# Kernel tuning notes

Hardware: AMD Instinct MI355X
Metric: run time of the kernel (lower is better)

## Reference

```python
import jax, jax.numpy as jnp
import numpy as np


def setup_inputs() -> dict:
    key = jax.random.key(0)
    k1, k2, k3, k4 = jax.random.split(key, 4)
    B, S, D = 2, 2048, 1024
    return {
        "X": jax.random.normal(k1, (B, S, D), dtype=jnp.float32),
        "W_q": jax.random.normal(k2, (D, D), dtype=jnp.float32),
        "W_k": jax.random.normal(k3, (D, D), dtype=jnp.float32),
        "W_v": jax.random.normal(k4, (D, D), dtype=jnp.float32),
        "n_heads": 16,
    }


def reference(X, W_q, W_k, W_v, n_heads):
    B, S, D = X.shape
    H = n_heads
    dh = D // H
    # QKV projections, split heads: [B,S,D] -> [H,B,S,dh]
    def split_heads(Y):
        return Y.reshape(B, S, H, dh).transpose(2, 0, 1, 3)
    Q = split_heads(X @ W_q)
    K = split_heads(X @ W_k)
    V = split_heads(X @ W_v)
    scale = 1.0 / jnp.sqrt(jnp.asarray(dh, dtype=X.dtype))
    # [H,B,S,S] attention scores (naive, matches the original)
    scores = jax.nn.softmax(jnp.einsum("hbqd,hbkd->hbqk", Q, K) * scale, axis=-1)
    out = jnp.einsum("hbqk,hbkd->hbqd", scores, V)  # [H,B,S,dh]
    # torch.concat(out, 0) over leading H dim -> [H*B, S, dh]
    return out.reshape(H * B, S, dh)
```

## Files before the change

kernel.cpp:

```cpp
#include <hip/hip_runtime.h>

typedef unsigned short u16;
typedef unsigned int u32;
typedef __bf16 bf16x8 __attribute__((ext_vector_type(8)));
typedef float f32x4 __attribute__((ext_vector_type(4)));
typedef float f32x16 __attribute__((ext_vector_type(16)));

extern "C" __device__ float __ocml_native_exp2_f32(float);

#define WT_HI_E  ((size_t)0)
#define WT_LO_E  ((size_t)3 << 20)
#define X_HI_E   ((size_t)6 << 20)
#define X_LO_E   ((size_t)10 << 20)
#define Q_HI_E   ((size_t)14 << 20)
#define Q_LO_E   ((size_t)18 << 20)
#define K_HI_E   ((size_t)22 << 20)
#define K_LO_E   ((size_t)26 << 20)
#define V_HI_E   ((size_t)30 << 20)
#define ML_BYTE  (17u << 20)

__device__ __forceinline__ u16 bf16_rne(float x) {
  u32 u = __float_as_uint(x);
  u32 r = (u + 0x7fffu + ((u >> 16) & 1u)) >> 16;
  return (u16)r;
}
__device__ __forceinline__ float bf16_f(u16 h) {
  return __uint_as_float(((u32)h) << 16);
}
__device__ __forceinline__ u16 f2bf(float x) {
  __bf16 b = (__bf16)x;
  return __builtin_bit_cast(u16, b);
}

__device__ __forceinline__ void gload16(const u16* g, u16* l) {
  __builtin_amdgcn_global_load_lds(
      (const __attribute__((address_space(1))) void*)g,
      (__attribute__((address_space(3))) void*)l, 16, 0, 0);
}

__global__ __launch_bounds__(256) void k_split(const float* __restrict__ X,
                                               const float* __restrict__ w0,
                                               const float* __restrict__ w1,
                                               const float* __restrict__ w2,
                                               u16* __restrict__ ws) {
  int bid = blockIdx.x;
  if (bid < 2048) {
    u16* xh = ws + X_HI_E;
    u16* xl = ws + X_LO_E;
    size_t i = ((size_t)bid * 256 + threadIdx.x) * 8;
    float4 a = *(const float4*)(X + i);
    float4 b = *(const float4*)(X + i + 4);
    float v[8] = {a.x, a.y, a.z, a.w, b.x, b.y, b.z, b.w};
    u32 Hh[4], Ll[4];
#pragma unroll
    for (int j = 0; j < 4; j++) {
      u16 h0 = f2bf(v[2 * j]);
      u16 h1 = f2bf(v[2 * j + 1]);
      u16 l0 = f2bf(v[2 * j] - bf16_f(h0));
      u16 l1 = f2bf(v[2 * j + 1] - bf16_f(h1));
      Hh[j] = (u32)h0 | ((u32)h1 << 16);
      Ll[j] = (u32)l0 | ((u32)l1 << 16);
    }
    *(uint4*)(xh + i) = make_uint4(Hh[0], Hh[1], Hh[2], Hh[3]);
    *(uint4*)(xl + i) = make_uint4(Ll[0], Ll[1], Ll[2], Ll[3]);
  } else {
    int wb = bid - 2048;
    int z = wb >> 8;
    int rem = wb & 255;
    int by = (rem >> 4) * 64, bx = (rem & 15) * 64;
    const float* W = (z == 0) ? w0 : ((z == 1) ? w1 : w2);
    u16* th = ws + WT_HI_E + (size_t)z * (1u << 20);
    u16* tl = ws + WT_LO_E + (size_t)z * (1u << 20);
    __shared__ float tile[64][65];
    int tx = threadIdx.x & 15, ty = threadIdx.x >> 4;
#pragma unroll
    for (int i = 0; i < 4; i++) {
      int r = ty + i * 16;
      float4 v = *(const float4*)(W + (size_t)(by + r) * 1024 + bx + tx * 4);
      tile[r][tx * 4 + 0] = v.x;
      tile[r][tx * 4 + 1] = v.y;
      tile[r][tx * 4 + 2] = v.z;
      tile[r][tx * 4 + 3] = v.w;
    }
    __syncthreads();
#pragma unroll
    for (int p = 0; p < 2; p++) {
      int t = threadIdx.x + 256 * p;
      int kc = t & 7, nl = t >> 3;
      u32 Hh[4], Ll[4];
#pragma unroll
      for (int u = 0; u < 4; u++) {
        float v0 = tile[kc * 8 + 2 * u][nl];
        float v1 = tile[kc * 8 + 2 * u + 1][nl];
        u16 h0 = f2bf(v0);
        u16 h1 = f2bf(v1);
        u16 l0 = f2bf(v0 - bf16_f(h0));
        u16 l1 = f2bf(v1 - bf16_f(h1));
        Hh[u] = (u32)h0 | ((u32)h1 << 16);
        Ll[u] = (u32)l0 | ((u32)l1 << 16);
      }
      size_t o = (size_t)(bx + nl) * 1024 + by + kc * 8;
      *(uint4*)(th + o) = make_uint4(Hh[0], Hh[1], Hh[2], Hh[3]);
      *(uint4*)(tl + o) = make_uint4(Ll[0], Ll[1], Ll[2], Ll[3]);
    }
  }
}

__global__ __launch_bounds__(256, 4) void k_proj(u16* __restrict__ ws) {
  int id = blockIdx.x;
  int xcd = id & 7;
  int loc = id >> 3;
  int m_loc = loc & 7;
  int rest = loc >> 3;
  int n_blk = rest & 7, z = rest >> 3;
  int M0 = (xcd * 8 + m_loc) * 64;
  int N0 = n_blk * 128;

  const u16* Xh = ws + X_HI_E;
  const u16* Xl = ws + X_LO_E;
  const u16* Wh = ws + WT_HI_E + (size_t)z * (1u << 20);
  const u16* Wl = ws + WT_LO_E + (size_t)z * (1u << 20);
  u16* dsth = ws + ((z == 0) ? Q_HI_E : ((z == 1) ? K_HI_E : V_HI_E));
  u16* dstl = (z == 0) ? (ws + Q_LO_E) : ((z == 1) ? (ws + K_LO_E) : (u16*)0);

  __shared__ u16 smem[12288];
  u16* sXh = smem;
  u16* sXl = smem + 2048;
  u16* sWh = smem + 4096;
  u16* sWl = smem + 8192;

  int tid = threadIdx.x, lane = tid & 63, w = tid >> 6;
  int quad = lane >> 4, l16 = lane & 15;
  int mb = (w & 1) * 32, nb = (w >> 1) * 64;

  const f32x4 z4 = {0.f, 0.f, 0.f, 0.f};
  f32x4 acc[4][2];
#pragma unroll
  for (int j = 0; j < 4; j++)
#pragma unroll
    for (int i = 0; i < 2; i++) acc[j][i] = z4;

  int xrow = tid >> 2, xq8 = tid & 3;

  for (int kk = 0; kk < 1024; kk += 32) {
    __syncthreads();
    {
      size_t gx = (size_t)(M0 + xrow) * 1024 + kk + xq8 * 8;
      gload16(Xh + gx, &sXh[(size_t)(w * 16) * 32]);
      if (z != 2) gload16(Xl + gx, &sXl[(size_t)(w * 16) * 32]);
#pragma unroll
      for (int j = 0; j < 2; j++) {
        int c = tid + 256 * j;
        int row = c >> 2, q8 = c & 3;
        size_t gw = (size_t)(N0 + row) * 1024 + kk + q8 * 8;
        gload16(Wh + gw, &sWh[(size_t)(j * 64 + w * 16) * 32]);
        if (z != 2) gload16(Wl + gw, &sWl[(size_t)(j * 64 + w * 16) * 32]);
      }
    }
    __syncthreads();
    bf16x8 ah[2], bh[4];
#pragma unroll
    for (int i = 0; i < 2; i++)
      ah[i] = *(const bf16x8*)&sXh[(mb + i * 16 + l16) * 32 + quad * 8];
#pragma unroll
    for (int j = 0; j < 4; j++)
      bh[j] = *(const bf16x8*)&sWh[(nb + j * 16 + l16) * 32 + quad * 8];
    if (z != 2) {
      bf16x8 al[2], bl[4];
#pragma unroll
      for (int i = 0; i < 2; i++)
        al[i] = *(const bf16x8*)&sXl[(mb + i * 16 + l16) * 32 + quad * 8];
#pragma unroll
      for (int j = 0; j < 4; j++)
        bl[j] = *(const bf16x8*)&sWl[(nb + j * 16 + l16) * 32 + quad * 8];
#pragma unroll
      for (int j = 0; j < 4; j++)
#pragma unroll
        for (int i = 0; i < 2; i++) {
          f32x4 c0 = acc[j][i];
          c0 = __builtin_amdgcn_mfma_f32_16x16x32_bf16(bh[j], ah[i], c0, 0, 0, 0);
          c0 = __builtin_amdgcn_mfma_f32_16x16x32_bf16(bh[j], al[i], c0, 0, 0, 0);
          c0 = __builtin_amdgcn_mfma_f32_16x16x32_bf16(bl[j], ah[i], c0, 0, 0, 0);
          acc[j][i] = c0;
        }
    } else {
#pragma unroll
      for (int j = 0; j < 4; j++)
#pragma unroll
        for (int i = 0; i < 2; i++)
          acc[j][i] = __builtin_amdgcn_mfma_f32_16x16x32_bf16(ah[i], bh[j], acc[j][i], 0, 0, 0);
    }
  }

  __syncthreads();
  int b = M0 >> 11, S0 = M0 & 2047;

  if (z != 2) {
    u16* my = smem + (size_t)w * 2048;
    int hh = (N0 + nb) >> 6;
    int sbase = S0 + mb;
    float qscale = (z == 0) ? (0.125f * 1.4426950408889634f) : 1.0f;
#pragma unroll
    for (int pass = 0; pass < 2; pass++) {
      u16* dst = pass ? dstl : dsth;
#pragma unroll
      for (int j = 0; j < 4; j++)
#pragma unroll
        for (int i = 0; i < 2; i++) {
          int dl = j * 16 + quad * 4;
          int sl = i * 16 + l16;
          u16 e[4];
#pragma unroll
          for (int r = 0; r < 4; r++) {
            float y = acc[j][i][r] * qscale;
            u16 hv = bf16_rne(y);
            e[r] = pass ? bf16_rne(y - bf16_f(hv)) : hv;
          }
          int elem = sl * 64 + (((dl >> 3) ^ (sl & 7)) << 3) + (dl & 7);
          *(uint2*)&my[elem] = make_uint2((u32)e[0] | ((u32)e[1] << 16),
                                          (u32)e[2] | ((u32)e[3] << 16));
        }
#pragma unroll
      for (int t = 0; t < 4; t++) {
        int sr = (lane >> 3) + t * 8;
        int p = lane & 7;
        int rc = (z == 1) ? p : (p ^ (sr & 7));
        uint4 v = *(const uint4*)&my[sr * 64 + rc * 8];
        size_t o = ((size_t)(hh * 2 + b) * 2048 + sbase + sr) * 64 + p * 8;
        *(uint4*)&dst[o] = v;
      }
    }
  } else {
#pragma unroll
    for (int j = 0; j < 4; j++)
#pragma unroll
      for (int i = 0; i < 2; i++) {
        int dl = j * 16 + l16;
        int s64 = mb + i * 16 + quad * 4;
        u16 e[4];
#pragma unroll
        for (int r = 0; r < 4; r++) e[r] = bf16_rne(acc[j][i][r]);
        int cp = ((s64 >> 3) & 7) ^ (dl & 7);
        int elem = (w >> 1) * 4096 + dl * 64 + (cp << 3) + (s64 & 7);
        *(uint2*)&smem[elem] = make_uint2((u32)e[0] | ((u32)e[1] << 16),
                                          (u32)e[2] | ((u32)e[3] << 16));
      }
    __syncthreads();
    int half = w >> 1;
    int hh = (N0 + half * 64) >> 6;
#pragma unroll
    for (int t = 0; t < 4; t++) {
      int dr = (w & 1) * 32 + (lane >> 3) + t * 8;
      int p = lane & 7;
      uint4 v = *(const uint4*)&smem[half * 4096 + dr * 64 + p * 8];
      size_t o = ((size_t)(hh * 2 + b) * 64 + dr) * 2048 + S0 + p * 8;
      *(uint4*)&dsth[o] = v;
    }
  }
}

__global__ __launch_bounds__(256, 3) void k_attn(u16* __restrict__ ws,
                                                 float* __restrict__ out) {
  const u16* Qh = ws + Q_HI_E;
  const u16* Ql = ws + Q_LO_E;
  const u16* Kh = ws + K_HI_E;
  const u16* Kl = ws + K_LO_E;
  const u16* Vt = ws + V_HI_E;

  __shared__ u16 sKh[2][64][64], sKl[2][64][64], sVt[2][64][64];

  int id = blockIdx.x;
  int hb = id & 31, qb = (id >> 5) & 15, half = id >> 9;
  int kbase = half << 10;
  int tid = threadIdx.x, w = tid >> 6, lane = tid & 63;
  int l31 = lane & 31, h = lane >> 5;
  size_t base = (size_t)hb * (2048 * 64);
  int qw0 = qb * 128 + w * 32;

  int srow = lane >> 3, sch = lane & 7;

  auto stage = [&](int buf, int t) {
    int kt = kbase + t * 64;
#pragma unroll
    for (int b2 = 0; b2 < 2; b2++) {
      int rr = w * 16 + b2 * 8;
      size_t kg = base + (size_t)(kt + rr + srow) * 64 + sch * 8;
      gload16(Kh + kg, &sKh[buf][rr][0]);
      gload16(Kl + kg, &sKl[buf][rr][0]);
      size_t vg = base + (size_t)(rr + srow) * 2048 + kt + sch * 8;
      gload16(Vt + vg, &sVt[buf][rr][0]);
    }
  };

  stage(0, 0);

  bf16x8 qh[4], ql[4];
#pragma unroll
  for (int ks = 0; ks < 4; ks++) {
    size_t off = base + (size_t)(qw0 + l31) * 64 + ks * 16 + h * 8;
    qh[ks] = *(const bf16x8*)(Qh + off);
    ql[ks] = *(const bf16x8*)(Ql + off);
  }

  f32x16 o[2];
#pragma unroll
  for (int i = 0; i < 16; i++) { o[0][i] = 0.f; o[1][i] = 0.f; }
  float mr = -1e30f, lr = 0.f;

  auto rdA = [&](const u16 t[64][64], int mt, int ks) -> bf16x8 {
    int ch = ((ks * 2 + h) ^ (l31 & 7)) * 8;
    return *(const bf16x8*)&t[mt * 32 + l31][ch];
  };

  for (int it = 0; it < 16; it++) {
    __syncthreads();
    if (it + 1 < 16) stage((it + 1) & 1, it + 1);
    int buf = it & 1;

    f32x16 sc[2];
#pragma unroll
    for (int i = 0; i < 16; i++) { sc[0][i] = 0.f; sc[1][i] = 0.f; }
#pragma unroll
    for (int ks = 0; ks < 4; ks++)
#pragma unroll
      for (int mt = 0; mt < 2; mt++) {
        bf16x8 kh = rdA(sKh[buf], mt, ks);
        bf16x8 kl = rdA(sKl[buf], mt, ks);
        sc[mt] = __builtin_amdgcn_mfma_f32_32x32x16_bf16(kh, qh[ks], sc[mt], 0, 0, 0);
        sc[mt] = __builtin_amdgcn_mfma_f32_32x32x16_bf16(kh, ql[ks], sc[mt], 0, 0, 0);
        sc[mt] = __builtin_amdgcn_mfma_f32_32x32x16_bf16(kl, qh[ks], sc[mt], 0, 0, 0);
      }

    float mx = sc[0][0];
#pragma unroll
    for (int i = 0; i < 16; i++) {
      mx = fmaxf(mx, sc[0][i]);
      mx = fmaxf(mx, sc[1][i]);
    }
    mx = fmaxf(mx, __shfl_xor(mx, 32));
    float mnew = fmaxf(mr, mx);
    float alpha = __ocml_native_exp2_f32(mr - mnew);
    mr = mnew;
    float rs = 0.f;
    u32 pk[2][8];
#pragma unroll
    for (int t = 0; t < 2; t++)
#pragma unroll
      for (int i = 0; i < 8; i++) {
        float p0 = __ocml_native_exp2_f32(sc[t][2 * i] - mnew);
        float p1 = __ocml_native_exp2_f32(sc[t][2 * i + 1] - mnew);
        rs += p0 + p1;
        u32 a = __float_as_uint(p0) + 0x8000u;
        u32 b = __float_as_uint(p1) + 0x8000u;
        pk[t][i] = __builtin_amdgcn_perm(b, a, 0x07060302u);
      }
    rs += __shfl_xor(rs, 32);
    lr = lr * alpha + rs;
#pragma unroll
    for (int i = 0; i < 16; i++) {
      o[0][i] *= alpha;
      o[1][i] *= alpha;
    }

#pragma unroll
    for (int ks = 0; ks < 4; ks++) {
      int t = ks >> 1, c = ks & 1;
      u32 b0 = pk[t][c * 4 + 0], b1 = pk[t][c * 4 + 1];
      u32 b2 = pk[t][c * 4 + 2], b3 = pk[t][c * 4 + 3];
      u32 rA = (u32)__shfl_xor((int)(h ? b0 : b2), 32);
      u32 rB = (u32)__shfl_xor((int)(h ? b1 : b3), 32);
      uint4 fb = h ? make_uint4(rA, rB, b2, b3) : make_uint4(b0, b1, rA, rB);
      bf16x8 pfrag = *(bf16x8*)&fb;
#pragma unroll
      for (int mt = 0; mt < 2; mt++) {
        bf16x8 vb = rdA(sVt[buf], mt, ks);
        o[mt] = __builtin_amdgcn_mfma_f32_32x32x16_bf16(vb, pfrag, o[mt], 0, 0, 0);
      }
    }
  }

  float* dst = (half == 0) ? out : (float*)ws;
  size_t grow = (size_t)hb * 2048 + qw0 + l31;
#pragma unroll
  for (int mt = 0; mt < 2; mt++)
#pragma unroll
    for (int g2 = 0; g2 < 4; g2++) {
      int d0 = mt * 32 + g2 * 8 + 4 * h;
      float4 v = make_float4(o[mt][g2 * 4 + 0], o[mt][g2 * 4 + 1],
                             o[mt][g2 * 4 + 2], o[mt][g2 * 4 + 3]);
      *(float4*)(dst + grow * 64 + d0) = v;
    }
  if (h == 0) {
    float2* ml = (float2*)((char*)ws + ML_BYTE);
    ml[(size_t)half * 65536 + grow] = make_float2(mr, lr);
  }
}

__global__ __launch_bounds__(256) void k_merge(u16* __restrict__ ws,
                                               float* __restrict__ out) {
  size_t g = (size_t)blockIdx.x * 256 + threadIdx.x;
  size_t row = g >> 4;
  const float2* ml = (const float2*)((const char*)ws + ML_BYTE);
  float2 a = ml[row];
  float2 b = ml[65536 + row];
  float M = fmaxf(a.x, b.x);
  float e0 = __ocml_native_exp2_f32(a.x - M);
  float e1 = __ocml_native_exp2_f32(b.x - M);
  float winv = 1.f / (a.y * e0 + b.y * e1);
  float4 p0 = ((const float4*)out)[g];
  float4 p1 = ((const float4*)(const void*)ws)[g];
  float4 r = make_float4((p0.x * e0 + p1.x * e1) * winv,
                         (p0.y * e0 + p1.y * e1) * winv,
                         (p0.z * e0 + p1.z * e1) * winv,
                         (p0.w * e0 + p1.w * e1) * winv);
  ((float4*)out)[g] = r;
}

extern "C" void kernel_launch(void* const* d_in, const int* in_sizes, int n_in,
                              void* d_out, int out_size, void* d_ws, size_t ws_size,
                              hipStream_t stream) {
  const float* X = (const float*)d_in[0];
  const float* Wq = (const float*)d_in[1];
  const float* Wk = (const float*)d_in[2];
  const float* Wv = (const float*)d_in[3];
  u16* ws = (u16*)d_ws;
  float* out = (float*)d_out;

  k_split<<<dim3(2816), dim3(256), 0, stream>>>(X, Wq, Wk, Wv, ws);
  k_proj<<<dim3(1536), dim3(256), 0, stream>>>(ws);
  k_attn<<<dim3(1024), dim3(256), 0, stream>>>(ws, out);
  k_merge<<<dim3(4096), dim3(256), 0, stream>>>(ws, out);
}
```

Baseline: 241.8 us.

## Process two 32-row query subtiles per wave in attention kernel

Each wave now handles 64 query rows (two 32-row subtiles) instead of 32, so every K/V fragment read from shared memory feeds twice as many MFMAs. The block covers 256 query rows, the grid halves to 512 blocks, and the launch-bounds occupancy hint drops from 3 to 2 to make room for the doubled accumulator and score registers. The aim is less LDS traffic per MFMA and fewer redundant K/V tile loads from global memory. The costs are lower occupancy, higher register pressure, and fewer blocks to spread across the GPU's compute units.

```diff
diff --git a/kernel.cpp b/kernel.cpp
--- a/kernel.cpp
+++ b/kernel.cpp
@@ -259,7 +259,7 @@
   }
 }
 
-__global__ __launch_bounds__(256, 3) void k_attn(u16* __restrict__ ws,
+__global__ __launch_bounds__(256, 2) void k_attn(u16* __restrict__ ws,
                                                  float* __restrict__ out) {
   const u16* Qh = ws + Q_HI_E;
   const u16* Ql = ws + Q_LO_E;
@@ -270,12 +270,12 @@
   __shared__ u16 sKh[2][64][64], sKl[2][64][64], sVt[2][64][64];
 
   int id = blockIdx.x;
-  int hb = id & 31, qb = (id >> 5) & 15, half = id >> 9;
+  int hb = id & 31, qb = (id >> 5) & 7, half = id >> 8;
   int kbase = half << 10;
   int tid = threadIdx.x, w = tid >> 6, lane = tid & 63;
   int l31 = lane & 31, h = lane >> 5;
   size_t base = (size_t)hb * (2048 * 64);
-  int qw0 = qb * 128 + w * 32;
+  int qw0 = qb * 256 + w * 64;
 
   int srow = lane >> 3, sch = lane & 7;
 
@@ -294,18 +294,23 @@
 
   stage(0, 0);
 
-  bf16x8 qh[4], ql[4];
-#pragma unroll
-  for (int ks = 0; ks < 4; ks++) {
-    size_t off = base + (size_t)(qw0 + l31) * 64 + ks * 16 + h * 8;
-    qh[ks] = *(const bf16x8*)(Qh + off);
-    ql[ks] = *(const bf16x8*)(Ql + off);
-  }
-
-  f32x16 o[2];
-#pragma unroll
-  for (int i = 0; i < 16; i++) { o[0][i] = 0.f; o[1][i] = 0.f; }
-  float mr = -1e30f, lr = 0.f;
+  bf16x8 qh[2][4], ql[2][4];
+#pragma unroll
+  for (int qs = 0; qs < 2; qs++)
+#pragma unroll
+    for (int ks = 0; ks < 4; ks++) {
+      size_t off = base + (size_t)(qw0 + qs * 32 + l31) * 64 + ks * 16 + h * 8;
+      qh[qs][ks] = *(const bf16x8*)(Qh + off);
+      ql[qs][ks] = *(const bf16x8*)(Ql + off);
+    }
+
+  f32x16 o[2][2];
+#pragma unroll
+  for (int qs = 0; qs < 2; qs++)
+#pragma unroll
+    for (int i = 0; i < 16; i++) { o[qs][0][i] = 0.f; o[qs][1][i] = 0.f; }
+  float mr[2] = {-1e30f, -1e30f};
+  float lr[2] = {0.f, 0.f};
 
   auto rdA = [&](const u16 t[64][64], int mt, int ks) -> bf16x8 {
     int ch = ((ks * 2 + h) ^ (l31 & 7)) * 8;
@@ -317,82 +322,96 @@
     if (it + 1 < 16) stage((it + 1) & 1, it + 1);
     int buf = it & 1;
 
-    f32x16 sc[2];
-#pragma unroll
-    for (int i = 0; i < 16; i++) { sc[0][i] = 0.f; sc[1][i] = 0.f; }
+    f32x16 sc[2][2];
+#pragma unroll
+    for (int qs = 0; qs < 2; qs++)
+#pragma unroll
+      for (int i = 0; i < 16; i++) { sc[qs][0][i] = 0.f; sc[qs][1][i] = 0.f; }
 #pragma unroll
     for (int ks = 0; ks < 4; ks++)
 #pragma unroll
       for (int mt = 0; mt < 2; mt++) {
         bf16x8 kh = rdA(sKh[buf], mt, ks);
         bf16x8 kl = rdA(sKl[buf], mt, ks);
-        sc[mt] = __builtin_amdgcn_mfma_f32_32x32x16_bf16(kh, qh[ks], sc[mt], 0, 0, 0);
-        sc[mt] = __builtin_amdgcn_mfma_f32_32x32x16_bf16(kh, ql[ks], sc[mt], 0, 0, 0);
-        sc[mt] = __builtin_amdgcn_mfma_f32_32x32x16_bf16(kl, qh[ks], sc[mt], 0, 0, 0);
-      }
-
-    float mx = sc[0][0];
-#pragma unroll
-    for (int i = 0; i < 16; i++) {
-      mx = fmaxf(mx, sc[0][i]);
-      mx = fmaxf(mx, sc[1][i]);
-    }
-    mx = fmaxf(mx, __shfl_xor(mx, 32));
-    float mnew = fmaxf(mr, mx);
-    float alpha = __ocml_native_exp2_f32(mr - mnew);
-    mr = mnew;
-    float rs = 0.f;
-    u32 pk[2][8];
-#pragma unroll
-    for (int t = 0; t < 2; t++)
-#pragma unroll
-      for (int i = 0; i < 8; i++) {
-        float p0 = __ocml_native_exp2_f32(sc[t][2 * i] - mnew);
-        float p1 = __ocml_native_exp2_f32(sc[t][2 * i + 1] - mnew);
-        rs += p0 + p1;
-        u32 a = __float_as_uint(p0) + 0x8000u;
-        u32 b = __float_as_uint(p1) + 0x8000u;
-        pk[t][i] = __builtin_amdgcn_perm(b, a, 0x07060302u);
-      }
-    rs += __shfl_xor(rs, 32);
-    lr = lr * alpha + rs;
-#pragma unroll
-    for (int i = 0; i < 16; i++) {
-      o[0][i] *= alpha;
-      o[1][i] *= alpha;
+        sc[0][mt] = __builtin_amdgcn_mfma_f32_32x32x16_bf16(kh, qh[0][ks], sc[0][mt], 0, 0, 0);
+        sc[1][mt] = __builtin_amdgcn_mfma_f32_32x32x16_bf16(kh, qh[1][ks], sc[1][mt], 0, 0, 0);
+        sc[0][mt] = __builtin_amdgcn_mfma_f32_32x32x16_bf16(kh, ql[0][ks], sc[0][mt], 0, 0, 0);
+        sc[1][mt] = __builtin_amdgcn_mfma_f32_32x32x16_bf16(kh, ql[1][ks], sc[1][mt], 0, 0, 0);
+        sc[0][mt] = __builtin_amdgcn_mfma_f32_32x32x16_bf16(kl, qh[0][ks], sc[0][mt], 0, 0, 0);
+        sc[1][mt] = __builtin_amdgcn_mfma_f32_32x32x16_bf16(kl, qh[1][ks], sc[1][mt], 0, 0, 0);
+      }
+
+    u32 pk[2][2][8];
+#pragma unroll
+    for (int qs = 0; qs < 2; qs++) {
+      float mx = sc[qs][0][0];
+#pragma unroll
+      for (int i = 0; i < 16; i++) {
+        mx = fmaxf(mx, sc[qs][0][i]);
+        mx = fmaxf(mx, sc[qs][1][i]);
+      }
+      mx = fmaxf(mx, __shfl_xor(mx, 32));
+      float mnew = fmaxf(mr[qs], mx);
+      float alpha = __ocml_native_exp2_f32(mr[qs] - mnew);
+      mr[qs] = mnew;
+      float rs = 0.f;
+#pragma unroll
+      for (int t = 0; t < 2; t++)
+#pragma unroll
+        for (int i = 0; i < 8; i++) {
+          float p0 = __ocml_native_exp2_f32(sc[qs][t][2 * i] - mnew);
+          float p1 = __ocml_native_exp2_f32(sc[qs][t][2 * i + 1] - mnew);
+          rs += p0 + p1;
+          u32 a = __float_as_uint(p0) + 0x8000u;
+          u32 b = __float_as_uint(p1) + 0x8000u;
+          pk[qs][t][i] = __builtin_amdgcn_perm(b, a, 0x07060302u);
+        }
+      rs += __shfl_xor(rs, 32);
+      lr[qs] = lr[qs] * alpha + rs;
+#pragma unroll
+      for (int i = 0; i < 16; i++) {
+        o[qs][0][i] *= alpha;
+        o[qs][1][i] *= alpha;
+      }
     }
 
 #pragma unroll
     for (int ks = 0; ks < 4; ks++) {
       int t = ks >> 1, c = ks & 1;
-      u32 b0 = pk[t][c * 4 + 0], b1 = pk[t][c * 4 + 1];
-      u32 b2 = pk[t][c * 4 + 2], b3 = pk[t][c * 4 + 3];
-      u32 rA = (u32)__shfl_xor((int)(h ? b0 : b2), 32);
-      u32 rB = (u32)__shfl_xor((int)(h ? b1 : b3), 32);
-      uint4 fb = h ? make_uint4(rA, rB, b2, b3) : make_uint4(b0, b1, rA, rB);
-      bf16x8 pfrag = *(bf16x8*)&fb;
+      bf16x8 pf[2];
+#pragma unroll
+      for (int qs = 0; qs < 2; qs++) {
+        u32 b0 = pk[qs][t][c * 4 + 0], b1 = pk[qs][t][c * 4 + 1];
+        u32 b2 = pk[qs][t][c * 4 + 2], b3 = pk[qs][t][c * 4 + 3];
+        u32 rA = (u32)__shfl_xor((int)(h ? b0 : b2), 32);
+        u32 rB = (u32)__shfl_xor((int)(h ? b1 : b3), 32);
+        uint4 fb = h ? make_uint4(rA, rB, b2, b3) : make_uint4(b0, b1, rA, rB);
+        pf[qs] = *(bf16x8*)&fb;
+      }
 #pragma unroll
       for (int mt = 0; mt < 2; mt++) {
         bf16x8 vb = rdA(sVt[buf], mt, ks);
-        o[mt] = __builtin_amdgcn_mfma_f32_32x32x16_bf16(vb, pfrag, o[mt], 0, 0, 0);
+        o[0][mt] = __builtin_amdgcn_mfma_f32_32x32x16_bf16(vb, pf[0], o[0][mt], 0, 0, 0);
+        o[1][mt] = __builtin_amdgcn_mfma_f32_32x32x16_bf16(vb, pf[1], o[1][mt], 0, 0, 0);
       }
     }
   }
 
   float* dst = (half == 0) ? out : (float*)ws;
-  size_t grow = (size_t)hb * 2048 + qw0 + l31;
-#pragma unroll
-  for (int mt = 0; mt < 2; mt++)
-#pragma unroll
-    for (int g2 = 0; g2 < 4; g2++) {
-      int d0 = mt * 32 + g2 * 8 + 4 * h;
-      float4 v = make_float4(o[mt][g2 * 4 + 0], o[mt][g2 * 4 + 1],
-                             o[mt][g2 * 4 + 2], o[mt][g2 * 4 + 3]);
-      *(float4*)(dst + grow * 64 + d0) = v;
-    }
-  if (h == 0) {
-    float2* ml = (float2*)((char*)ws + ML_BYTE);
-    ml[(size_t)half * 65536 + grow] = make_float2(mr, lr);
+  float2* ml = (float2*)((char*)ws + ML_BYTE);
+#pragma unroll
+  for (int qs = 0; qs < 2; qs++) {
+    size_t grow = (size_t)hb * 2048 + qw0 + qs * 32 + l31;
+#pragma unroll
+    for (int mt = 0; mt < 2; mt++)
+#pragma unroll
+      for (int g2 = 0; g2 < 4; g2++) {
+        int d0 = mt * 32 + g2 * 8 + 4 * h;
+        float4 v = make_float4(o[qs][mt][g2 * 4 + 0], o[qs][mt][g2 * 4 + 1],
+                               o[qs][mt][g2 * 4 + 2], o[qs][mt][g2 * 4 + 3]);
+        *(float4*)(dst + grow * 64 + d0) = v;
+      }
+    if (h == 0) ml[(size_t)half * 65536 + grow] = make_float2(mr[qs], lr[qs]);
   }
 }
 
@@ -428,6 +447,6 @@
 
   k_split<<<dim3(2816), dim3(256), 0, stream>>>(X, Wq, Wk, Wv, ws);
   k_proj<<<dim3(1536), dim3(256), 0, stream>>>(ws);
-  k_attn<<<dim3(1024), dim3(256), 0, stream>>>(ws, out);
+  k_attn<<<dim3(512), dim3(256), 0, stream>>>(ws, out);
   k_merge<<<dim3(4096), dim3(256), 0, stream>>>(ws, out);
 }
```

Result: no change. 240.0 us (-0.8%).
